# Optimization experiments

Hardware: AMD Instinct MI355X
Metric: run time of the kernel (lower is better)

The kernel has to match this reference:

```python
import jax, jax.numpy as jnp
import numpy as np

WEIGHT = 1.0
TEMPERATURE = 1.0
POWER = 2.0
NEG_FILL = -1e9
EPS = 1e-8


def _cos_sim_matrix(x):
    # row-normalize then GEMM: equivalent to pairwise F.cosine_similarity
    norms = jnp.linalg.norm(x, axis=-1, keepdims=True)
    xn = x / jnp.maximum(norms, EPS)
    return xn @ xn.T  # [N, N]


def setup_inputs() -> dict:
    key = jax.random.key(0)
    k1, k2 = jax.random.split(key)
    model_output = jax.random.normal(k1, (8192, 512), dtype=jnp.float32)
    targets = jax.random.normal(k2, (8192, 768), dtype=jnp.float32)
    return {"model_output": model_output, "targets": targets}


def reference(model_output, targets):
    N = model_output.shape[0]
    eye = jnp.eye(N, dtype=bool)

    sim_o = jnp.where(eye, NEG_FILL, _cos_sim_matrix(model_output))
    sim_t = jnp.where(eye, NEG_FILL, _cos_sim_matrix(targets))

    student_log_probs = jax.nn.log_softmax(sim_o / TEMPERATURE, axis=-1)
    teacher_probs = jax.nn.softmax(sim_t / TEMPERATURE, axis=-1)

    weights = jax.lax.stop_gradient(teacher_probs ** POWER)

    # torch F.kl_div(input=log_p_student, target=p_teacher, reduction='none')
    # = where(target > 0, target * (log(target) - input), 0)
    tp_safe = jnp.where(teacher_probs > 0, teacher_probs, 1.0)
    kl = jnp.where(teacher_probs > 0,
                   teacher_probs * (jnp.log(tp_safe) - student_log_probs),
                   0.0)

    loss = jnp.mean(weights * kl)
    return WEIGHT * loss
```

## Files before the change

### kernel.cpp

```cpp
#include <hip/hip_runtime.h>

#define N    8192
#define DT   768
#define DO   512
#define BM   128
#define BN   128
#define TI   (N / BM)
#define TJ   (N / BN)
#define NTILE (TI * (TI + 1) / 2)
#define NSLOT (2 * TJ)
#define PL    ((size_t)NSLOT * N)
#define NKT   (DT / 32)
#define NKO   (DO / 32)

typedef __attribute__((ext_vector_type(8))) short   short8;
typedef __attribute__((ext_vector_type(4))) float   floatx4;

struct alignas(8) us4 { unsigned short x[4]; };

__device__ inline unsigned short f2bf(float x) {
    union { float f; unsigned int u; } v; v.f = x;
    unsigned int r = v.u + 0x7fffu + ((v.u >> 16) & 1u);
    return (unsigned short)(r >> 16);
}
__device__ inline float bf2f(unsigned short u) {
    union { unsigned int u; float f; } v; v.u = ((unsigned int)u) << 16;
    return v.f;
}

__device__ inline void gl2lds16(const unsigned short* g, unsigned short* l) {
    __builtin_amdgcn_global_load_lds(
        (const __attribute__((address_space(1))) unsigned int*)(const void*)g,
        (__attribute__((address_space(3))) unsigned int*)(void*)l,
        16, 0, 0);
}

template <int D>
__device__ inline void stage_tile(const unsigned short* __restrict__ X,
                                  unsigned short* sAb, unsigned short* sBb,
                                  int i0, int j0, int k, int t) {
    #pragma unroll
    for (int h = 0; h < 2; ++h) {
        const int idx = t + h * 256;
        const int r   = idx >> 2;
        const int cs  = ((idx & 3) ^ ((r >> 1) & 3)) << 3;
        gl2lds16(X + (size_t)(i0 + r) * D + k + cs, &sAb[idx * 8]);
        gl2lds16(X + (size_t)(j0 + r) * D + k + cs, &sBb[idx * 8]);
    }
}

__device__ inline void mfma_step(const unsigned short* __restrict__ sAb,
                                 const unsigned short* __restrict__ sBb,
                                 floatx4 (&acc)[4][4],
                                 int wm, int wn, int lr, int lgx) {
    short8 af[4], bf[4];
    #pragma unroll
    for (int mi = 0; mi < 4; ++mi)
        af[mi] = *(const short8*)&sAb[(wm * 64 + mi * 16 + lr) * 32 + (lgx << 3)];
    #pragma unroll
    for (int ni = 0; ni < 4; ++ni)
        bf[ni] = *(const short8*)&sBb[(wn * 64 + ni * 16 + lr) * 32 + (lgx << 3)];
    #pragma unroll
    for (int mi = 0; mi < 4; ++mi)
        #pragma unroll
        for (int ni = 0; ni < 4; ++ni)
            acc[mi][ni] = __builtin_amdgcn_mfma_f32_16x16x32_bf16(
                af[mi], bf[ni], acc[mi][ni], 0, 0, 0);
}

__device__ inline void tile_coords(int bid, int& ti, int& tj) {
    const int swb = (bid & 7) * (NTILE / 8) + (bid >> 3);
    int rem = swb; int a = 0;
    while (rem >= TI - a) { rem -= TI - a; ++a; }
    ti = a; tj = a + rem;
}

__global__ void norm_kernel(const float* __restrict__ Tg,
                            const float* __restrict__ Mo,
                            unsigned short* __restrict__ Xt,
                            unsigned short* __restrict__ Xo,
                            float* __restrict__ zero_me) {
    if (blockIdx.x == 0 && threadIdx.x == 0) zero_me[0] = 0.0f;
    int bid = blockIdx.x;
    const float* X; unsigned short* Xn; int D;
    if (bid < N / 4) { X = Tg; Xn = Xt; D = DT; }
    else             { bid -= N / 4; X = Mo; Xn = Xo; D = DO; }
    const int row  = bid * 4 + (threadIdx.x >> 6);
    const int lane = threadIdx.x & 63;
    const int nch  = D >> 8;
    const float* xr = X + (size_t)row * D;
    floatx4 vc[3];
    float ss = 0.0f;
    #pragma unroll
    for (int h = 0; h < 3; ++h) {
        if (h < nch) {
            vc[h] = *(const floatx4*)(xr + lane * 4 + h * 256);
            ss += vc[h][0] * vc[h][0] + vc[h][1] * vc[h][1]
                + vc[h][2] * vc[h][2] + vc[h][3] * vc[h][3];
        }
    }
    #pragma unroll
    for (int m = 32; m >= 1; m >>= 1) ss += __shfl_xor(ss, m);
    const float scale = 1.0f / fmaxf(sqrtf(ss), 1e-8f);
    unsigned short* outr = Xn + (size_t)row * D;
    #pragma unroll
    for (int h = 0; h < 3; ++h) {
        if (h < nch) {
            us4 o;
            #pragma unroll
            for (int j = 0; j < 4; ++j) o.x[j] = f2bf(vc[h][j] * scale);
            *(us4*)(outr + lane * 4 + h * 256) = o;
        }
    }
}

__launch_bounds__(256, 3)
__global__ void fused_t_kernel(const unsigned short* __restrict__ Xt,
                               float* __restrict__ partials,
                               unsigned int* __restrict__ Wws) {
    __shared__ unsigned short sA[3][BM * 32];
    __shared__ unsigned short sB[3][BN * 32];

    const int t    = threadIdx.x;
    const int lane = t & 63;
    const int w    = t >> 6;
    const int wm   = w >> 1, wn = w & 1;
    const int lr   = lane & 15, lg = lane >> 4;
    const int lgx  = lg ^ ((lr >> 1) & 3);

    int ti, tj; tile_coords(blockIdx.x, ti, tj);
    const bool offdiag = (ti != tj);
    const int i0 = ti * BM, j0 = tj * BN;
    unsigned int* const wt = Wws + (size_t)blockIdx.x * 8192;

    floatx4 acc[4][4];
    #pragma unroll
    for (int a = 0; a < 4; ++a)
        #pragma unroll
        for (int b = 0; b < 4; ++b)
            acc[a][b] = (floatx4){0.0f, 0.0f, 0.0f, 0.0f};

    stage_tile<DT>(Xt, sA[0], sB[0], i0, j0, 0, t);
    stage_tile<DT>(Xt, sA[1], sB[1], i0, j0, 32, t);

    for (int s = 0; s < NKT; ++s) {
        if (s + 1 < NKT) asm volatile("s_waitcnt vmcnt(4)" ::: "memory");
        else             asm volatile("s_waitcnt vmcnt(0)" ::: "memory");
        __builtin_amdgcn_s_barrier();
        asm volatile("" ::: "memory");
        if (s + 2 < NKT)
            stage_tile<DT>(Xt, sA[(s + 2) % 3], sB[(s + 2) % 3], i0, j0, (s + 2) * 32, t);
        mfma_step(sA[s % 3], sB[s % 3], acc, wm, wn, lr, lgx);
        asm volatile("" ::: "memory");
    }

    {
        float czt[4], cvv[4], cua[4];
        #pragma unroll
        for (int ni = 0; ni < 4; ++ni) { czt[ni] = 0.0f; cvv[ni] = 0.0f; cua[ni] = 0.0f; }
        #pragma unroll
        for (int mi = 0; mi < 4; ++mi) {
            unsigned int wpk[4][2];
            #pragma unroll
            for (int r = 0; r < 4; ++r) {
                const int row = wm * 64 + mi * 16 + lg * 4 + r;
                const int gi  = i0 + row;
                float zt = 0.0f, vv = 0.0f, ua = 0.0f;
                #pragma unroll
                for (int ni = 0; ni < 4; ++ni) {
                    const int gj = j0 + wn * 64 + ni * 16 + lr;
                    const float a = acc[mi][ni][r];
                    float ea = __expf(a - 1.0f);
                    if (gi == gj) ea = 0.0f;
                    const float e3 = ea * ea * ea;
                    zt += ea; vv += e3; ua += e3 * a;
                    czt[ni] += ea; cvv[ni] += e3; cua[ni] += e3 * a;
                    if ((r & 1) == 0) wpk[ni][r >> 1]  = (unsigned int)f2bf(e3);
                    else              wpk[ni][r >> 1] |= ((unsigned int)f2bf(e3)) << 16;
                }
                #pragma unroll
                for (int m = 8; m >= 1; m >>= 1) {
                    zt += __shfl_xor(zt, m);
                    vv += __shfl_xor(vv, m);
                    ua += __shfl_xor(ua, m);
                }
                if (lr == 0) {
                    const size_t base = (size_t)(tj * 2 + wn) * N + gi;
                    partials[0 * PL + base] = zt;
                    partials[1 * PL + base] = vv;
                    partials[2 * PL + base] = ua;
                }
            }
            #pragma unroll
            for (int ni = 0; ni < 4; ++ni)
                #pragma unroll
                for (int rp = 0; rp < 2; ++rp)
                    wt[(mi * 8 + ni * 2 + rp) * 256 + t] = wpk[ni][rp];
        }
        if (offdiag) {
            #pragma unroll
            for (int ni = 0; ni < 4; ++ni) {
                #pragma unroll
                for (int m = 16; m <= 32; m <<= 1) {
                    czt[ni] += __shfl_xor(czt[ni], m);
                    cvv[ni] += __shfl_xor(cvv[ni], m);
                    cua[ni] += __shfl_xor(cua[ni], m);
                }
            }
            if (lg == 0) {
                #pragma unroll
                for (int ni = 0; ni < 4; ++ni) {
                    const int gj = j0 + wn * 64 + ni * 16 + lr;
                    const size_t base = (size_t)(ti * 2 + wm) * N + gj;
                    partials[0 * PL + base] = czt[ni];
                    partials[1 * PL + base] = cvv[ni];
                    partials[2 * PL + base] = cua[ni];
                }
            }
        }
    }
}

__launch_bounds__(256, 3)
__global__ void fused_o_kernel(const unsigned short* __restrict__ Xo,
                               float* __restrict__ partials,
                               const unsigned int* __restrict__ Wws) {
    __shared__ unsigned short sA[3][BM * 32];
    __shared__ unsigned short sB[3][BN * 32];

    const int t    = threadIdx.x;
    const int lane = t & 63;
    const int w    = t >> 6;
    const int wm   = w >> 1, wn = w & 1;
    const int lr   = lane & 15, lg = lane >> 4;
    const int lgx  = lg ^ ((lr >> 1) & 3);

    int ti, tj; tile_coords(blockIdx.x, ti, tj);
    const bool offdiag = (ti != tj);
    const int i0 = ti * BM, j0 = tj * BN;
    const unsigned int* const wt = Wws + (size_t)blockIdx.x * 8192;

    floatx4 acc[4][4];
    #pragma unroll
    for (int a = 0; a < 4; ++a)
        #pragma unroll
        for (int b = 0; b < 4; ++b)
            acc[a][b] = (floatx4){0.0f, 0.0f, 0.0f, 0.0f};

    stage_tile<DO>(Xo, sA[0], sB[0], i0, j0, 0, t);
    stage_tile<DO>(Xo, sA[1], sB[1], i0, j0, 32, t);

    for (int s = 0; s < NKO; ++s) {
        if (s + 1 < NKO) asm volatile("s_waitcnt vmcnt(4)" ::: "memory");
        else             asm volatile("s_waitcnt vmcnt(0)" ::: "memory");
        __builtin_amdgcn_s_barrier();
        asm volatile("" ::: "memory");
        if (s + 2 < NKO)
            stage_tile<DO>(Xo, sA[(s + 2) % 3], sB[(s + 2) % 3], i0, j0, (s + 2) * 32, t);
        mfma_step(sA[s % 3], sB[s % 3], acc, wm, wn, lr, lgx);
        asm volatile("" ::: "memory");
    }

    {
        unsigned int wld[32];
        #pragma unroll
        for (int pi = 0; pi < 32; ++pi)
            wld[pi] = wt[pi * 256 + t];
        float czo[4], cwb[4];
        #pragma unroll
        for (int ni = 0; ni < 4; ++ni) { czo[ni] = 0.0f; cwb[ni] = 0.0f; }
        #pragma unroll
        for (int mi = 0; mi < 4; ++mi) {
            #pragma unroll
            for (int r = 0; r < 4; ++r) {
                const int row = wm * 64 + mi * 16 + lg * 4 + r;
                const int gi  = i0 + row;
                float zo = 0.0f, wb = 0.0f;
                #pragma unroll
                for (int ni = 0; ni < 4; ++ni) {
                    const int gj = j0 + wn * 64 + ni * 16 + lr;
                    const float b = acc[mi][ni][r];
                    float eb = __expf(b - 1.0f);
                    if (gi == gj) eb = 0.0f;
                    const unsigned int pw = wld[mi * 8 + ni * 2 + (r >> 1)];
                    const float wgt = bf2f((unsigned short)((r & 1) ? (pw >> 16)
                                                                    : (pw & 0xffffu)));
                    zo += eb; wb += wgt * b;
                    czo[ni] += eb; cwb[ni] += wgt * b;
                }
                #pragma unroll
                for (int m = 8; m >= 1; m >>= 1) {
                    zo += __shfl_xor(zo, m);
                    wb += __shfl_xor(wb, m);
                }
                if (lr == 0) {
                    const size_t base = (size_t)(tj * 2 + wn) * N + gi;
                    partials[3 * PL + base] = zo;
                    partials[4 * PL + base] = wb;
                }
            }
        }
        if (offdiag) {
            #pragma unroll
            for (int ni = 0; ni < 4; ++ni) {
                #pragma unroll
                for (int m = 16; m <= 32; m <<= 1) {
                    czo[ni] += __shfl_xor(czo[ni], m);
                    cwb[ni] += __shfl_xor(cwb[ni], m);
                }
            }
            if (lg == 0) {
                #pragma unroll
                for (int ni = 0; ni < 4; ++ni) {
                    const int gj = j0 + wn * 64 + ni * 16 + lr;
                    const size_t base = (size_t)(ti * 2 + wm) * N + gj;
                    partials[3 * PL + base] = czo[ni];
                    partials[4 * PL + base] = cwb[ni];
                }
            }
        }
    }
}

__global__ void reduce_kernel(const float* __restrict__ partials,
                              float* __restrict__ out) {
    __shared__ float sh[5][256];
    const int t    = threadIdx.x;
    const int lane = t & 63;
    const int g    = t >> 6;
    const int i    = blockIdx.x * 64 + lane;
    float s[5] = {0.0f, 0.0f, 0.0f, 0.0f, 0.0f};
    for (int jb = g * (NSLOT / 4); jb < (g + 1) * (NSLOT / 4); ++jb) {
        const size_t base = (size_t)jb * N + i;
        #pragma unroll
        for (int p = 0; p < 5; ++p) s[p] += partials[p * PL + base];
    }
    #pragma unroll
    for (int p = 0; p < 5; ++p) sh[p][t] = s[p];
    __syncthreads();
    if (g == 0) {
        float v[5];
        #pragma unroll
        for (int p = 0; p < 5; ++p)
            v[p] = sh[p][lane] + sh[p][64 + lane] + sh[p][128 + lane] + sh[p][192 + lane];
        float li = (v[2] - v[4] + v[1] * __logf(v[3] / v[0])) / (v[0] * v[0] * v[0]);
        #pragma unroll
        for (int m = 32; m >= 1; m >>= 1) li += __shfl_xor(li, m);
        if (lane == 0)
            atomicAdd(out, li * (1.0f / ((float)N * (float)N)));
    }
}

extern "C" void kernel_launch(void* const* d_in, const int* in_sizes, int n_in,
                              void* d_out, int out_size, void* d_ws, size_t ws_size,
                              hipStream_t stream) {
    (void)in_sizes; (void)n_in; (void)out_size; (void)ws_size;
    const float* mo = (const float*)d_in[0];
    const float* tg = (const float*)d_in[1];
    float* out = (float*)d_out;

    char* ws = (char*)d_ws;
    unsigned short* Xt = (unsigned short*)ws;
    unsigned short* Xo = (unsigned short*)(ws + (size_t)N * DT * 2);
    float* partials    = (float*)(ws + (size_t)N * DT * 2 + (size_t)N * DO * 2);
    unsigned int* Wws  = (unsigned int*)((char*)partials + 5 * PL * sizeof(float));

    norm_kernel<<<2 * (N / 4), 256, 0, stream>>>(tg, mo, Xt, Xo, out);
    fused_t_kernel<<<NTILE, 256, 0, stream>>>(Xt, partials, Wws);
    fused_o_kernel<<<NTILE, 256, 0, stream>>>(Xo, partials, Wws);
    reduce_kernel<<<N / 64, 256, 0, stream>>>(partials, out);
}
```

Baseline: 325.0 us.

## Enlarge tiles to 256x256 with 512 threads, deeper 4-stage pipeline and setprio

```diff
diff --git a/kernel.cpp b/kernel.cpp
--- a/kernel.cpp
+++ b/kernel.cpp
@@ -3,12 +3,12 @@
 #define N    8192
 #define DT   768
 #define DO   512
-#define BM   128
-#define BN   128
+#define BM   256
+#define BN   256
 #define TI   (N / BM)
 #define TJ   (N / BN)
 #define NTILE (TI * (TI + 1) / 2)
-#define NSLOT (2 * TJ)
+#define NSLOT 256
 #define PL    ((size_t)NSLOT * N)
 #define NKT   (DT / 32)
 #define NKO   (DO / 32)
@@ -41,7 +41,7 @@
                                   int i0, int j0, int k, int t) {
     #pragma unroll
     for (int h = 0; h < 2; ++h) {
-        const int idx = t + h * 256;
+        const int idx = t + h * 512;
         const int r   = idx >> 2;
         const int cs  = ((idx & 3) ^ ((r >> 1) & 3)) << 3;
         gl2lds16(X + (size_t)(i0 + r) * D + k + cs, &sAb[idx * 8]);
@@ -51,17 +51,17 @@
 
 __device__ inline void mfma_step(const unsigned short* __restrict__ sAb,
                                  const unsigned short* __restrict__ sBb,
-                                 floatx4 (&acc)[4][4],
+                                 floatx4 (&acc)[8][4],
                                  int wm, int wn, int lr, int lgx) {
-    short8 af[4], bf[4];
-    #pragma unroll
-    for (int mi = 0; mi < 4; ++mi)
-        af[mi] = *(const short8*)&sAb[(wm * 64 + mi * 16 + lr) * 32 + (lgx << 3)];
+    short8 af[8], bf[4];
+    #pragma unroll
+    for (int mi = 0; mi < 8; ++mi)
+        af[mi] = *(const short8*)&sAb[(wm * 128 + mi * 16 + lr) * 32 + (lgx << 3)];
     #pragma unroll
     for (int ni = 0; ni < 4; ++ni)
         bf[ni] = *(const short8*)&sBb[(wn * 64 + ni * 16 + lr) * 32 + (lgx << 3)];
     #pragma unroll
-    for (int mi = 0; mi < 4; ++mi)
+    for (int mi = 0; mi < 8; ++mi)
         #pragma unroll
         for (int ni = 0; ni < 4; ++ni)
             acc[mi][ni] = __builtin_amdgcn_mfma_f32_16x16x32_bf16(
@@ -114,56 +114,64 @@
     }
 }
 
-__launch_bounds__(256, 3)
+__launch_bounds__(512, 2)
 __global__ void fused_t_kernel(const unsigned short* __restrict__ Xt,
                                float* __restrict__ partials,
                                unsigned int* __restrict__ Wws) {
-    __shared__ unsigned short sA[3][BM * 32];
-    __shared__ unsigned short sB[3][BN * 32];
+    __shared__ unsigned short sA[4][BM * 32];
+    __shared__ unsigned short sB[4][BN * 32];
 
     const int t    = threadIdx.x;
     const int lane = t & 63;
     const int w    = t >> 6;
-    const int wm   = w >> 1, wn = w & 1;
+    const int wm   = w >> 2, wn = w & 3;
     const int lr   = lane & 15, lg = lane >> 4;
     const int lgx  = lg ^ ((lr >> 1) & 3);
 
     int ti, tj; tile_coords(blockIdx.x, ti, tj);
     const bool offdiag = (ti != tj);
     const int i0 = ti * BM, j0 = tj * BN;
-    unsigned int* const wt = Wws + (size_t)blockIdx.x * 8192;
-
-    floatx4 acc[4][4];
-    #pragma unroll
-    for (int a = 0; a < 4; ++a)
+    unsigned int* const wt = Wws + (size_t)blockIdx.x * 32768;
+
+    floatx4 acc[8][4];
+    #pragma unroll
+    for (int a = 0; a < 8; ++a)
         #pragma unroll
         for (int b = 0; b < 4; ++b)
             acc[a][b] = (floatx4){0.0f, 0.0f, 0.0f, 0.0f};
 
     stage_tile<DT>(Xt, sA[0], sB[0], i0, j0, 0, t);
     stage_tile<DT>(Xt, sA[1], sB[1], i0, j0, 32, t);
+    stage_tile<DT>(Xt, sA[2], sB[2], i0, j0, 64, t);
 
     for (int s = 0; s < NKT; ++s) {
-        if (s + 1 < NKT) asm volatile("s_waitcnt vmcnt(4)" ::: "memory");
-        else             asm volatile("s_waitcnt vmcnt(0)" ::: "memory");
+        if (s + 2 < NKT)      asm volatile("s_waitcnt vmcnt(8)" ::: "memory");
+        else if (s + 1 < NKT) asm volatile("s_waitcnt vmcnt(4)" ::: "memory");
+        else                  asm volatile("s_waitcnt vmcnt(0)" ::: "memory");
         __builtin_amdgcn_s_barrier();
         asm volatile("" ::: "memory");
-        if (s + 2 < NKT)
-            stage_tile<DT>(Xt, sA[(s + 2) % 3], sB[(s + 2) % 3], i0, j0, (s + 2) * 32, t);
-        mfma_step(sA[s % 3], sB[s % 3], acc, wm, wn, lr, lgx);
+        if (s + 3 < NKT)
+            stage_tile<DT>(Xt, sA[(s + 3) & 3], sB[(s + 3) & 3], i0, j0, (s + 3) * 32, t);
+        __builtin_amdgcn_s_setprio(1);
+        mfma_step(sA[s & 3], sB[s & 3], acc, wm, wn, lr, lgx);
+        __builtin_amdgcn_s_setprio(0);
         asm volatile("" ::: "memory");
     }
 
     {
-        float czt[4], cvv[4], cua[4];
-        #pragma unroll
-        for (int ni = 0; ni < 4; ++ni) { czt[ni] = 0.0f; cvv[ni] = 0.0f; cua[ni] = 0.0f; }
-        #pragma unroll
-        for (int mi = 0; mi < 4; ++mi) {
+        float czt[2][4], cvv[2][4], cua[2][4];
+        #pragma unroll
+        for (int hh = 0; hh < 2; ++hh)
+            #pragma unroll
+            for (int ni = 0; ni < 4; ++ni) {
+                czt[hh][ni] = 0.0f; cvv[hh][ni] = 0.0f; cua[hh][ni] = 0.0f;
+            }
+        #pragma unroll
+        for (int mi = 0; mi < 8; ++mi) {
             unsigned int wpk[4][2];
             #pragma unroll
             for (int r = 0; r < 4; ++r) {
-                const int row = wm * 64 + mi * 16 + lg * 4 + r;
+                const int row = wm * 128 + mi * 16 + lg * 4 + r;
                 const int gi  = i0 + row;
                 float zt = 0.0f, vv = 0.0f, ua = 0.0f;
                 #pragma unroll
@@ -174,7 +182,8 @@
                     if (gi == gj) ea = 0.0f;
                     const float e3 = ea * ea * ea;
                     zt += ea; vv += e3; ua += e3 * a;
-                    czt[ni] += ea; cvv[ni] += e3; cua[ni] += e3 * a;
+                    czt[mi >> 2][ni] += ea; cvv[mi >> 2][ni] += e3;
+                    cua[mi >> 2][ni] += e3 * a;
                     if ((r & 1) == 0) wpk[ni][r >> 1]  = (unsigned int)f2bf(e3);
                     else              wpk[ni][r >> 1] |= ((unsigned int)f2bf(e3)) << 16;
                 }
@@ -185,7 +194,7 @@
                     ua += __shfl_xor(ua, m);
                 }
                 if (lr == 0) {
-                    const size_t base = (size_t)(tj * 2 + wn) * N + gi;
+                    const size_t base = (size_t)(tj * 4 + wn) * N + gi;
                     partials[0 * PL + base] = zt;
                     partials[1 * PL + base] = vv;
                     partials[2 * PL + base] = ua;
@@ -195,128 +204,148 @@
             for (int ni = 0; ni < 4; ++ni)
                 #pragma unroll
                 for (int rp = 0; rp < 2; ++rp)
-                    wt[(mi * 8 + ni * 2 + rp) * 256 + t] = wpk[ni][rp];
+                    wt[(mi * 8 + ni * 2 + rp) * 512 + t] = wpk[ni][rp];
         }
         if (offdiag) {
             #pragma unroll
-            for (int ni = 0; ni < 4; ++ni) {
-                #pragma unroll
-                for (int m = 16; m <= 32; m <<= 1) {
-                    czt[ni] += __shfl_xor(czt[ni], m);
-                    cvv[ni] += __shfl_xor(cvv[ni], m);
-                    cua[ni] += __shfl_xor(cua[ni], m);
-                }
+            for (int hh = 0; hh < 2; ++hh)
+                #pragma unroll
+                for (int ni = 0; ni < 4; ++ni) {
+                    #pragma unroll
+                    for (int m = 16; m <= 32; m <<= 1) {
+                        czt[hh][ni] += __shfl_xor(czt[hh][ni], m);
+                        cvv[hh][ni] += __shfl_xor(cvv[hh][ni], m);
+                        cua[hh][ni] += __shfl_xor(cua[hh][ni], m);
+                    }
+                }
+            if (lg == 0) {
+                #pragma unroll
+                for (int hh = 0; hh < 2; ++hh)
+                    #pragma unroll
+                    for (int ni = 0; ni < 4; ++ni) {
+                        const int gj = j0 + wn * 64 + ni * 16 + lr;
+                        const size_t base =
+                            (size_t)(128 + ti * 4 + wm * 2 + hh) * N + gj;
+                        partials[0 * PL + base] = czt[hh][ni];
+                        partials[1 * PL + base] = cvv[hh][ni];
+                        partials[2 * PL + base] = cua[hh][ni];
+                    }
             }
-            if (lg == 0) {
-                #pragma unroll
-                for (int ni = 0; ni < 4; ++ni) {
-                    const int gj = j0 + wn * 64 + ni * 16 + lr;
-                    const size_t base = (size_t)(ti * 2 + wm) * N + gj;
-                    partials[0 * PL + base] = czt[ni];
-                    partials[1 * PL + base] = cvv[ni];
-                    partials[2 * PL + base] = cua[ni];
-                }
-            }
-        }
-    }
-}
-
-__launch_bounds__(256, 3)
+        }
+    }
+}
+
+__launch_bounds__(512, 2)
 __global__ void fused_o_kernel(const unsigned short* __restrict__ Xo,
                                float* __restrict__ partials,
                                const unsigned int* __restrict__ Wws) {
-    __shared__ unsigned short sA[3][BM * 32];
-    __shared__ unsigned short sB[3][BN * 32];
+    __shared__ unsigned short sA[4][BM * 32];
+    __shared__ unsigned short sB[4][BN * 32];
 
     const int t    = threadIdx.x;
     const int lane = t & 63;
     const int w    = t >> 6;
-    const int wm   = w >> 1, wn = w & 1;
+    const int wm   = w >> 2, wn = w & 3;
     const int lr   = lane & 15, lg = lane >> 4;
     const int lgx  = lg ^ ((lr >> 1) & 3);
 
     int ti, tj; tile_coords(blockIdx.x, ti, tj);
     const bool offdiag = (ti != tj);
     const int i0 = ti * BM, j0 = tj * BN;
-    const unsigned int* const wt = Wws + (size_t)blockIdx.x * 8192;
-
-    floatx4 acc[4][4];
-    #pragma unroll
-    for (int a = 0; a < 4; ++a)
+    const unsigned int* const wt = Wws + (size_t)blockIdx.x * 32768;
+
+    floatx4 acc[8][4];
+    #pragma unroll
+    for (int a = 0; a < 8; ++a)
         #pragma unroll
         for (int b = 0; b < 4; ++b)
             acc[a][b] = (floatx4){0.0f, 0.0f, 0.0f, 0.0f};
 
     stage_tile<DO>(Xo, sA[0], sB[0], i0, j0, 0, t);
     stage_tile<DO>(Xo, sA[1], sB[1], i0, j0, 32, t);
+    stage_tile<DO>(Xo, sA[2], sB[2], i0, j0, 64, t);
 
     for (int s = 0; s < NKO; ++s) {
-        if (s + 1 < NKO) asm volatile("s_waitcnt vmcnt(4)" ::: "memory");
-        else             asm volatile("s_waitcnt vmcnt(0)" ::: "memory");
+        if (s + 2 < NKO)      asm volatile("s_waitcnt vmcnt(8)" ::: "memory");
+        else if (s + 1 < NKO) asm volatile("s_waitcnt vmcnt(4)" ::: "memory");
+        else                  asm volatile("s_waitcnt vmcnt(0)" ::: "memory");
         __builtin_amdgcn_s_barrier();
         asm volatile("" ::: "memory");
-        if (s + 2 < NKO)
-            stage_tile<DO>(Xo, sA[(s + 2) % 3], sB[(s + 2) % 3], i0, j0, (s + 2) * 32, t);
-        mfma_step(sA[s % 3], sB[s % 3], acc, wm, wn, lr, lgx);
+        if (s + 3 < NKO)
+            stage_tile<DO>(Xo, sA[(s + 3) & 3], sB[(s + 3) & 3], i0, j0, (s + 3) * 32, t);
+        __builtin_amdgcn_s_setprio(1);
+        mfma_step(sA[s & 3], sB[s & 3], acc, wm, wn, lr, lgx);
+        __builtin_amdgcn_s_setprio(0);
         asm volatile("" ::: "memory");
     }
 
     {
-        unsigned int wld[32];
-        #pragma unroll
-        for (int pi = 0; pi < 32; ++pi)
-            wld[pi] = wt[pi * 256 + t];
-        float czo[4], cwb[4];
-        #pragma unroll
-        for (int ni = 0; ni < 4; ++ni) { czo[ni] = 0.0f; cwb[ni] = 0.0f; }
-        #pragma unroll
-        for (int mi = 0; mi < 4; ++mi) {
-            #pragma unroll
-            for (int r = 0; r < 4; ++r) {
-                const int row = wm * 64 + mi * 16 + lg * 4 + r;
-                const int gi  = i0 + row;
-                float zo = 0.0f, wb = 0.0f;
+        float czo[2][4], cwb[2][4];
+        #pragma unroll
+        for (int hh = 0; hh < 2; ++hh)
+            #pragma unroll
+            for (int ni = 0; ni < 4; ++ni) { czo[hh][ni] = 0.0f; cwb[hh][ni] = 0.0f; }
+        #pragma unroll
+        for (int half = 0; half < 2; ++half) {
+            unsigned int wld[32];
+            #pragma unroll
+            for (int pi = 0; pi < 32; ++pi)
+                wld[pi] = wt[(half * 32 + pi) * 512 + t];
+            #pragma unroll
+            for (int mq = 0; mq < 4; ++mq) {
+                const int mi = half * 4 + mq;
+                #pragma unroll
+                for (int r = 0; r < 4; ++r) {
+                    const int row = wm * 128 + mi * 16 + lg * 4 + r;
+                    const int gi  = i0 + row;
+                    float zo = 0.0f, wb = 0.0f;
+                    #pragma unroll
+                    for (int ni = 0; ni < 4; ++ni) {
+                        const int gj = j0 + wn * 64 + ni * 16 + lr;
+                        const float b = acc[mi][ni][r];
+                        float eb = __expf(b - 1.0f);
+                        if (gi == gj) eb = 0.0f;
+                        const unsigned int pw = wld[mq * 8 + ni * 2 + (r >> 1)];
+                        const float wgt = bf2f((unsigned short)((r & 1) ? (pw >> 16)
+                                                                        : (pw & 0xffffu)));
+                        zo += eb; wb += wgt * b;
+                        czo[half][ni] += eb; cwb[half][ni] += wgt * b;
+                    }
+                    #pragma unroll
+                    for (int m = 8; m >= 1; m >>= 1) {
+                        zo += __shfl_xor(zo, m);
+                        wb += __shfl_xor(wb, m);
+                    }
+                    if (lr == 0) {
+                        const size_t base = (size_t)(tj * 4 + wn) * N + gi;
+                        partials[3 * PL + base] = zo;
+                        partials[4 * PL + base] = wb;
+                    }
+                }
+            }
+        }
+        if (offdiag) {
+            #pragma unroll
+            for (int hh = 0; hh < 2; ++hh)
                 #pragma unroll
                 for (int ni = 0; ni < 4; ++ni) {
-                    const int gj = j0 + wn * 64 + ni * 16 + lr;
-                    const float b = acc[mi][ni][r];
-                    float eb = __expf(b - 1.0f);
-                    if (gi == gj) eb = 0.0f;
-                    const unsigned int pw = wld[mi * 8 + ni * 2 + (r >> 1)];
-                    const float wgt = bf2f((unsigned short)((r & 1) ? (pw >> 16)
-                                                                    : (pw & 0xffffu)));
-                    zo += eb; wb += wgt * b;
-                    czo[ni] += eb; cwb[ni] += wgt * b;
-                }
-                #pragma unroll
-                for (int m = 8; m >= 1; m >>= 1) {
-                    zo += __shfl_xor(zo, m);
-                    wb += __shfl_xor(wb, m);
-                }
-                if (lr == 0) {
-                    const size_t base = (size_t)(tj * 2 + wn) * N + gi;
-                    partials[3 * PL + base] = zo;
-                    partials[4 * PL + base] = wb;
-                }
-            }
-        }
-        if (offdiag) {
-            #pragma unroll
-            for (int ni = 0; ni < 4; ++ni) {
-                #pragma unroll
-                for (int m = 16; m <= 32; m <<= 1) {
-                    czo[ni] += __shfl_xor(czo[ni], m);
-                    cwb[ni] += __shfl_xor(cwb[ni], m);
-                }
-            }
+                    #pragma unroll
+                    for (int m = 16; m <= 32; m <<= 1) {
+                        czo[hh][ni] += __shfl_xor(czo[hh][ni], m);
+                        cwb[hh][ni] += __shfl_xor(cwb[hh][ni], m);
+                    }
+                }
             if (lg == 0) {
                 #pragma unroll
-                for (int ni = 0; ni < 4; ++ni) {
-                    const int gj = j0 + wn * 64 + ni * 16 + lr;
-                    const size_t base = (size_t)(ti * 2 + wm) * N + gj;
-                    partials[3 * PL + base] = czo[ni];
-                    partials[4 * PL + base] = cwb[ni];
-                }
+                for (int hh = 0; hh < 2; ++hh)
+                    #pragma unroll
+                    for (int ni = 0; ni < 4; ++ni) {
+                        const int gj = j0 + wn * 64 + ni * 16 + lr;
+                        const size_t base =
+                            (size_t)(128 + ti * 4 + wm * 2 + hh) * N + gj;
+                        partials[3 * PL + base] = czo[hh][ni];
+                        partials[4 * PL + base] = cwb[hh][ni];
+                    }
             }
         }
     }
@@ -329,9 +358,10 @@
     const int lane = t & 63;
     const int g    = t >> 6;
     const int i    = blockIdx.x * 64 + lane;
+    const int w0   = (blockIdx.x >> 2) * 4;
     float s[5] = {0.0f, 0.0f, 0.0f, 0.0f, 0.0f};
-    for (int jb = g * (NSLOT / 4); jb < (g + 1) * (NSLOT / 4); ++jb) {
-        const size_t base = (size_t)jb * N + i;
+    for (int u = g * 32; u < g * 32 + 32; ++u) {
+        const size_t base = (size_t)(w0 + u) * N + i;
         #pragma unroll
         for (int p = 0; p < 5; ++p) s[p] += partials[p * PL + base];
     }
@@ -366,7 +396,7 @@
     unsigned int* Wws  = (unsigned int*)((char*)partials + 5 * PL * sizeof(float));
 
     norm_kernel<<<2 * (N / 4), 256, 0, stream>>>(tg, mo, Xt, Xo, out);
-    fused_t_kernel<<<NTILE, 256, 0, stream>>>(Xt, partials, Wws);
-    fused_o_kernel<<<NTILE, 256, 0, stream>>>(Xo, partials, Wws);
+    fused_t_kernel<<<NTILE, 512, 0, stream>>>(Xt, partials, Wws);
+    fused_o_kernel<<<NTILE, 512, 0, stream>>>(Xo, partials, Wws);
     reduce_kernel<<<N / 64, 256, 0, stream>>>(partials, out);
 }
```

After: 622.2 us. 91.4% more time.
